# Optimization experiments

Hardware: AMD Instinct MI355X
Metric: run time of the kernel (lower is better)

Reference implementation:

```python
import jax, jax.numpy as jnp
import numpy as np

N = 50000          # num nodes
E = 1_000_000      # num edges
H = 64             # hidden_dim
IMG, TWT, NUMP, CAT = 512, 768, 16, 8
NCLS, NET = 2, 3   # num_classes, num_edge_types


def setup_inputs() -> dict:
    key = jax.random.key(0)
    ks = jax.random.split(key, 40)
    f32 = jnp.float32
    w = lambda k, s: (jax.random.normal(k, s, f32) * 0.02)
    inp = {
        # forward args
        "image": jax.random.normal(ks[0], (N, IMG), f32),
        "tweets": jax.random.normal(ks[1], (N, TWT), f32),
        "num_prop": jax.random.normal(ks[2], (N, NUMP), f32),
        "category": jax.random.normal(ks[3], (N, CAT), f32),
        "edge_index": jax.random.randint(ks[4], (2, E), 0, N, jnp.int32),
        "edge_type": jax.random.randint(ks[5], (E,), 0, NET, jnp.int32),
        # explicit randomness (replaces randn_like / Bernoulli.sample)
        "eps": jax.random.normal(ks[6], (E, H), f32),
        "u": jax.random.uniform(ks[7], (E,), f32),
        # parameters (stored [in, out]; y = x @ W + b)
        "Wi": w(ks[8], (IMG, H)), "bi": jnp.zeros((H,), f32),
        "Wt": w(ks[9], (TWT, H)), "bt": jnp.zeros((H,), f32),
        "Wn": w(ks[10], (NUMP, H)), "bn": jnp.zeros((H,), f32),
        "Wc": w(ks[11], (CAT, H)), "bc": jnp.zeros((H,), f32),
        "Wf": w(ks[12], (4 * H, H)), "bf": jnp.zeros((H,), f32),
        "Eet": w(ks[13], (NET, 2 * H)),              # edge_type_embed
        "Wmu": w(ks[14], (2 * H, H)), "bmu": jnp.zeros((H,), f32),
        "Wlv": w(ks[15], (2 * H, H)), "blv": jnp.zeros((H,), f32),
        "Wm1": w(ks[16], (2 * H, 64)), "bm1": jnp.zeros((64,), f32),
        "Wm2": w(ks[17], (64, 1)), "bm2": jnp.zeros((1,), f32),
        "Wcls": w(ks[18], (H, NCLS)), "bcls": jnp.zeros((NCLS,), f32),
    }
    return inp


def reference(image, tweets, num_prop, category, edge_index, edge_type, eps, u,
              Wi, bi, Wt, bt, Wn, bn, Wc, bc, Wf, bf, Eet,
              Wmu, bmu, Wlv, blv, Wm1, bm1, Wm2, bm2, Wcls, bcls):
    relu = jax.nn.relu
    # encode_user
    img_f = relu(image @ Wi + bi)
    twt_f = relu(tweets @ Wt + bt)
    num_f = relu(num_prop @ Wn + bn)
    cat_f = relu(category @ Wc + bc)
    node_features = relu(jnp.concatenate([img_f, twt_f, num_f, cat_f], -1) @ Wf + bf)  # [N, H]

    src, dst = edge_index[0], edge_index[1]
    u_i, u_j = node_features[src], node_features[dst]          # [E, H] each
    edge_emb = relu(jnp.concatenate([u_i, u_j], -1) + Eet[edge_type])  # [E, 2H]

    # parameterized_gaussian (z unused downstream, kept for fidelity)
    mu = edge_emb @ Wmu + bmu
    log_var = edge_emb @ Wlv + blv
    z = mu + eps * jnp.exp(0.5 * log_var)

    # edge confidence + Bernoulli sample via inverse-CDF with provided uniforms
    logits_e = (relu(edge_emb @ Wm1 + bm1) @ Wm2 + bm2)[:, 0]  # [E]
    p_ij = jax.nn.sigmoid(logits_e)
    s = (u < p_ij).astype(node_features.dtype)                 # trusted-edge indicator, [E]

    # segment-mean of dst features over trusted edges, grouped by src
    sums = jax.ops.segment_sum(u_j * s[:, None], src, num_segments=N)  # [N, H]
    cnt = jax.ops.segment_sum(s, src, num_segments=N)                  # [N]
    agg = jnp.where(cnt[:, None] > 0, sums / jnp.maximum(cnt, 1.0)[:, None], node_features)

    return agg @ Wcls + bcls  # [N, num_classes]
```

## Files before the change

### kernel.cpp

```cpp
#include <hip/hip_runtime.h>
#include <cstdint>

typedef short short8 __attribute__((ext_vector_type(8)));
typedef float f32x4  __attribute__((ext_vector_type(4)));

__device__ __forceinline__ void split2(float x, short& h, short& l) {
  unsigned u  = __float_as_uint(x);
  unsigned rh = u + 0x7FFFu + ((u >> 16) & 1u);
  h = (short)(rh >> 16);
  float hf = __uint_as_float((rh >> 16) << 16);
  float lf = x - hf;
  unsigned ul = __float_as_uint(lf);
  unsigned rl = ul + 0x7FFFu + ((ul >> 16) & 1u);
  l = (short)(rl >> 16);
}

__global__ __launch_bounds__(256) void init_head(int* __restrict__ head, int N)
{
  const int i = blockIdx.x * 256 + threadIdx.x;
  if (i < N) head[i] = -1;
}

__global__ __launch_bounds__(256) void prep_w(
    const float* __restrict__ Wi, const float* __restrict__ Wt,
    const float* __restrict__ Wn, const float* __restrict__ Wc,
    const float* __restrict__ Wf, short* __restrict__ hi, short* __restrict__ lo)
{
  int idx = blockIdx.x * 256 + threadIdx.x;
  if (idx >= 1600 * 64) return;
  int kp = idx >> 6, col = idx & 63;
  const float* W; int K, kloc, base;
  if (kp < 512)       { W = Wi; K = 512; kloc = kp;        base = 0;    }
  else if (kp < 1280) { W = Wt; K = 768; kloc = kp - 512;  base = 512;  }
  else if (kp < 1312) { W = Wn; K = 16;  kloc = kp - 1280; base = 1280; }
  else if (kp < 1344) { W = Wc; K = 8;   kloc = kp - 1312; base = 1312; }
  else                { W = Wf; K = 256; kloc = kp - 1344; base = 1344; }
  float x = (kloc < K) ? W[(size_t)kloc * 64 + col] : 0.f;
  short h, l; split2(x, h, l);
  int s = kloc >> 5;
  int addr = ((s * 4 + (col >> 4)) * 64 + ((col & 15) | (((kloc >> 3) & 3) << 4))) * 8 + (kloc & 7);
  size_t o = (size_t)base * 64 + addr;
  hi[o] = h; lo[o] = l;
}

__global__ __launch_bounds__(256) void gemm_mfma_relu(
    const float* __restrict__ A, int lda, int K, int ksteps,
    const short* __restrict__ Whi, const short* __restrict__ Wlo,
    const float* __restrict__ bias, float* __restrict__ C, int ldc, int M)
{
  __shared__ short Ahi[2][2048];
  __shared__ short Alo[2][2048];
  const int tid = threadIdx.x;
  const int m0  = blockIdx.x * 64;
  const int w   = tid >> 6, l = tid & 63;

  f32x4 acc[4];
#pragma unroll
  for (int n = 0; n < 4; n++) acc[n] = (f32x4){0.f, 0.f, 0.f, 0.f};

  const int srow = tid >> 3;
  const int k0   = (tid & 7) * 4;
  const int i0   = k0 & 7;
  const int kg   = k0 >> 3;

  auto stage = [&](int s, int buf) {
#pragma unroll
    for (int r2 = 0; r2 < 2; r2++) {
      const int row  = srow + r2 * 32;
      const int grow = m0 + row;
      const int k    = s * 32 + k0;
      float4 a = make_float4(0.f, 0.f, 0.f, 0.f);
      if (grow < M && k < K)
        a = *reinterpret_cast<const float4*>(A + (size_t)grow * lda + k);
      unsigned hp0, hp1, lp0, lp1;
      asm("v_cvt_pk_bf16_f32 %0, %1, %2" : "=v"(hp0) : "v"(a.x), "v"(a.y));
      asm("v_cvt_pk_bf16_f32 %0, %1, %2" : "=v"(hp1) : "v"(a.z), "v"(a.w));
      float h0 = __uint_as_float(hp0 << 16);
      float h1 = __uint_as_float(hp0 & 0xFFFF0000u);
      float h2 = __uint_as_float(hp1 << 16);
      float h3 = __uint_as_float(hp1 & 0xFFFF0000u);
      float l0 = a.x - h0, l1 = a.y - h1, l2 = a.z - h2, l3 = a.w - h3;
      asm("v_cvt_pk_bf16_f32 %0, %1, %2" : "=v"(lp0) : "v"(l0), "v"(l1));
      asm("v_cvt_pk_bf16_f32 %0, %1, %2" : "=v"(lp1) : "v"(l2), "v"(l3));
      const int addr = (row >> 4) * 512 + (((row & 15) | (kg << 4)) * 8 + i0);
      *reinterpret_cast<uint2*>(&Ahi[buf][addr]) = make_uint2(hp0, hp1);
      *reinterpret_cast<uint2*>(&Alo[buf][addr]) = make_uint2(lp0, lp1);
    }
  };

  stage(0, 0);
  for (int s = 0; s < ksteps; s++) {
    __syncthreads();
    if (s + 1 < ksteps) stage(s + 1, (s + 1) & 1);
    const int buf = s & 1;
    short8 ahi = *reinterpret_cast<const short8*>(&Ahi[buf][w * 512 + l * 8]);
    short8 alo = *reinterpret_cast<const short8*>(&Alo[buf][w * 512 + l * 8]);
#pragma unroll
    for (int n = 0; n < 4; n++) {
      short8 whi = *reinterpret_cast<const short8*>(&Whi[((size_t)(s * 4 + n)) * 512 + l * 8]);
      short8 wlo = *reinterpret_cast<const short8*>(&Wlo[((size_t)(s * 4 + n)) * 512 + l * 8]);
      acc[n] = __builtin_amdgcn_mfma_f32_16x16x32_bf16(ahi, whi, acc[n], 0, 0, 0);
      acc[n] = __builtin_amdgcn_mfma_f32_16x16x32_bf16(alo, whi, acc[n], 0, 0, 0);
      acc[n] = __builtin_amdgcn_mfma_f32_16x16x32_bf16(ahi, wlo, acc[n], 0, 0, 0);
    }
  }

  const int rb  = m0 + w * 16 + (l >> 4) * 4;
  const int c15 = l & 15;
#pragma unroll
  for (int n = 0; n < 4; n++) {
    const int c = n * 16 + c15;
    const float bb = bias[c];
#pragma unroll
    for (int j = 0; j < 4; j++) {
      const int r = rb + j;
      if (r < M) C[(size_t)r * ldc + c] = fmaxf(acc[n][j] + bb, 0.f);
    }
  }
}

__global__ __launch_bounds__(256) void build_table(
    const float* __restrict__ nf, const float* __restrict__ Eet, int eoff,
    const float* __restrict__ Wm1half, const float* __restrict__ bias,
    float* __restrict__ Tab, int N3)
{
  __shared__ float Es[64][68];
  __shared__ float Ws[64][68];
  const int tid = threadIdx.x;
  const int m0  = blockIdx.x * 64;
  const int ty  = tid >> 4, tx = tid & 15;

  {
    const int r = tid >> 2;
    const int rg = m0 + r;
    const int n = rg / 3;
    const int t = rg - n * 3;
#pragma unroll
    for (int j = 0; j < 4; j++) {
      const int k0 = (tid & 3) * 4 + j * 16;
      float4 v = make_float4(0.f, 0.f, 0.f, 0.f);
      if (rg < N3) {
        float4 x = *reinterpret_cast<const float4*>(nf + (size_t)n * 64 + k0);
        float4 e = *reinterpret_cast<const float4*>(Eet + (size_t)t * 128 + eoff + k0);
        v.x = fmaxf(x.x + e.x, 0.f); v.y = fmaxf(x.y + e.y, 0.f);
        v.z = fmaxf(x.z + e.z, 0.f); v.w = fmaxf(x.w + e.w, 0.f);
      }
      Es[k0 + 0][r] = v.x; Es[k0 + 1][r] = v.y;
      Es[k0 + 2][r] = v.z; Es[k0 + 3][r] = v.w;
    }
  }
  {
    const int kr = tid >> 4, c0 = (tid & 15) * 4;
#pragma unroll
    for (int j = 0; j < 4; j++) {
      const int k = kr + j * 16;
      *reinterpret_cast<float4*>(&Ws[k][c0]) =
          *reinterpret_cast<const float4*>(Wm1half + (size_t)k * 64 + c0);
    }
  }
  __syncthreads();

  float acc[4][4];
#pragma unroll
  for (int i = 0; i < 4; i++)
#pragma unroll
    for (int j = 0; j < 4; j++) acc[i][j] = 0.f;

#pragma unroll 16
  for (int kk = 0; kk < 64; kk++) {
    float4 a = *reinterpret_cast<const float4*>(&Es[kk][ty * 4]);
    float4 w = *reinterpret_cast<const float4*>(&Ws[kk][tx * 4]);
    float av[4] = {a.x, a.y, a.z, a.w};
    float wv[4] = {w.x, w.y, w.z, w.w};
#pragma unroll
    for (int i = 0; i < 4; i++)
#pragma unroll
      for (int j = 0; j < 4; j++)
        acc[i][j] = fmaf(av[i], wv[j], acc[i][j]);
  }

  float4 bv = make_float4(0.f, 0.f, 0.f, 0.f);
  if (bias) bv = *reinterpret_cast<const float4*>(bias + tx * 4);
#pragma unroll
  for (int i = 0; i < 4; i++) {
    const int row = m0 + ty * 4 + i;
    if (row < N3) {
      float4 o = make_float4(acc[i][0] + bv.x, acc[i][1] + bv.y,
                             acc[i][2] + bv.z, acc[i][3] + bv.w);
      *reinterpret_cast<float4*>(Tab + (size_t)row * 64 + tx * 4) = o;
    }
  }
}

__global__ __launch_bounds__(256) void edge_kernel(
    const int* __restrict__ ei, const int* __restrict__ et,
    const float* __restrict__ u,
    const float* __restrict__ Atab, const float* __restrict__ Btab,
    const float* __restrict__ Wm2, const float* __restrict__ bm2,
    int* __restrict__ head, int* __restrict__ nxt, int E)
{
  const int tid = threadIdx.x;
  const int e   = blockIdx.x * 16 + (tid >> 4);
  const int sub = tid & 15;
  if (e >= E) return;

  const int sn = ei[e];
  const int dn = ei[E + e];
  const int t  = et[e];

  float4 a  = *reinterpret_cast<const float4*>(Atab + ((size_t)sn * 3 + t) * 64 + sub * 4);
  float4 b  = *reinterpret_cast<const float4*>(Btab + ((size_t)dn * 3 + t) * 64 + sub * 4);
  float4 wv = *reinterpret_cast<const float4*>(Wm2 + sub * 4);

  float v = fmaxf(a.x + b.x, 0.f) * wv.x;
  v = fmaf(fmaxf(a.y + b.y, 0.f), wv.y, v);
  v = fmaf(fmaxf(a.z + b.z, 0.f), wv.z, v);
  v = fmaf(fmaxf(a.w + b.w, 0.f), wv.w, v);
  v += __shfl_xor(v, 1);
  v += __shfl_xor(v, 2);
  v += __shfl_xor(v, 4);
  v += __shfl_xor(v, 8);

  if (sub == 0) {
    const float p = 1.f / (1.f + expf(-(v + bm2[0])));
    if (u[e] < p) {
      nxt[e] = atomicExch(&head[sn], e);
    }
  }
}

__global__ __launch_bounds__(256) void node_kernel(
    const int* __restrict__ head, const int* __restrict__ nxt,
    const int* __restrict__ ei,
    const float* __restrict__ nf,
    const float* __restrict__ Wcls, const float* __restrict__ bcls,
    float* __restrict__ out, int N, int E)
{
  const int n    = (int)((blockIdx.x * (unsigned)blockDim.x + threadIdx.x) >> 6);
  const int lane = threadIdx.x & 63;
  if (n >= N) return;

  float acc = 0.f;
  int   c   = 0;
  int   e   = head[n];
  while (e >= 0) {
    const int dn = ei[E + e];
    acc += nf[(size_t)dn * 64 + lane];
    c++;
    e = nxt[e];
  }

  const float agg = (c > 0) ? acc / (float)c : nf[(size_t)n * 64 + lane];
  float r0 = agg * Wcls[lane * 2 + 0];
  float r1 = agg * Wcls[lane * 2 + 1];
#pragma unroll
  for (int off = 32; off; off >>= 1) {
    r0 += __shfl_xor(r0, off, 64);
    r1 += __shfl_xor(r1, off, 64);
  }
  if (lane == 0) {
    out[(size_t)n * 2 + 0] = r0 + bcls[0];
    out[(size_t)n * 2 + 1] = r1 + bcls[1];
  }
}

extern "C" void kernel_launch(void* const* d_in, const int* in_sizes, int n_in,
                              void* d_out, int out_size, void* d_ws, size_t ws_size,
                              hipStream_t stream)
{
  const float* image    = (const float*)d_in[0];
  const float* tweets   = (const float*)d_in[1];
  const float* num_prop = (const float*)d_in[2];
  const float* category = (const float*)d_in[3];
  const int*   ei       = (const int*)  d_in[4];
  const int*   et       = (const int*)  d_in[5];
  const float* u        = (const float*)d_in[7];
  const float* Wi  = (const float*)d_in[8],  *bi  = (const float*)d_in[9];
  const float* Wt  = (const float*)d_in[10], *bt  = (const float*)d_in[11];
  const float* Wn  = (const float*)d_in[12], *bn  = (const float*)d_in[13];
  const float* Wc  = (const float*)d_in[14], *bc  = (const float*)d_in[15];
  const float* Wf  = (const float*)d_in[16], *bf  = (const float*)d_in[17];
  const float* Eet = (const float*)d_in[18];
  const float* Wm1 = (const float*)d_in[23], *bm1 = (const float*)d_in[24];
  const float* Wm2 = (const float*)d_in[25], *bm2 = (const float*)d_in[26];
  const float* Wcls= (const float*)d_in[27], *bcls= (const float*)d_in[28];
  float* out = (float*)d_out;

  const int N = in_sizes[0] / 512;
  const int E = in_sizes[5];

  float* ws = (float*)d_ws;
  size_t off = 0;
  float* concat = ws + off;  off += (size_t)N * 256;
  float* nf     = ws + off;  off += (size_t)N * 64;
  float* Atab   = ws + off;  off += (size_t)N * 3 * 64;
  float* Btab   = ws + off;  off += (size_t)N * 3 * 64;
  int*   head   = (int*)(ws + off);  off += (size_t)N;
  int*   nxt    = (int*)(ws + off);  off += (size_t)E;
  short* Wfhi   = (short*)(ws + off);  off += (1600 * 64) / 2;
  short* Wflo   = (short*)(ws + off);  off += (1600 * 64) / 2;

  init_head<<<(N + 255) / 256, 256, 0, stream>>>(head, N);

  prep_w<<<(1600 * 64 + 255) / 256, 256, 0, stream>>>(Wi, Wt, Wn, Wc, Wf, Wfhi, Wflo);

  const int gN = (N + 63) / 64;
  gemm_mfma_relu<<<gN, 256, 0, stream>>>(image,    512, 512, 16, Wfhi + (size_t)0    * 64, Wflo + (size_t)0    * 64, bi, concat + 0,   256, N);
  gemm_mfma_relu<<<gN, 256, 0, stream>>>(tweets,   768, 768, 24, Wfhi + (size_t)512  * 64, Wflo + (size_t)512  * 64, bt, concat + 64,  256, N);
  gemm_mfma_relu<<<gN, 256, 0, stream>>>(num_prop, 16,  16,  1,  Wfhi + (size_t)1280 * 64, Wflo + (size_t)1280 * 64, bn, concat + 128, 256, N);
  gemm_mfma_relu<<<gN, 256, 0, stream>>>(category, 8,   8,   1,  Wfhi + (size_t)1312 * 64, Wflo + (size_t)1312 * 64, bc, concat + 192, 256, N);
  gemm_mfma_relu<<<gN, 256, 0, stream>>>(concat,   256, 256, 8,  Wfhi + (size_t)1344 * 64, Wflo + (size_t)1344 * 64, bf, nf,           64,  N);

  const int N3 = N * 3;
  const int gT = (N3 + 63) / 64;
  build_table<<<gT, 256, 0, stream>>>(nf, Eet, 0,  Wm1,           bm1,     Atab, N3);
  build_table<<<gT, 256, 0, stream>>>(nf, Eet, 64, Wm1 + 64 * 64, nullptr, Btab, N3);

  edge_kernel<<<(E + 15) / 16, 256, 0, stream>>>(ei, et, u, Atab, Btab,
                                                 Wm2, bm2, head, nxt, E);

  node_kernel<<<(N + 3) / 4, 256, 0, stream>>>(head, nxt, ei, nf, Wcls, bcls,
                                               out, N, E);
}
```

Measured before the change: 391.6 us.

## Fuse encoder GEMMs into one kernel and move edge tables to split-bf16 MFMA

The four input-projection GEMMs and the fusion GEMM are merged into one encoder kernel. Each segment's ReLU output is kept in shared memory and immediately multiplied into the fusion accumulator, so the N×256 concat buffer is never written to or read back from global memory. The two FP32 build_table launches become one MFMA kernel using split-bf16 weights prepared by prep_w. The node aggregation also switches to double accumulation for accuracy, which costs FP64 adds in the gather loop.

```diff
diff --git a/kernel.cpp b/kernel.cpp
--- a/kernel.cpp
+++ b/kernel.cpp
@@ -15,6 +15,21 @@
   l = (short)(rl >> 16);
 }
 
+__device__ __forceinline__ void split4(float4 a, uint2& hp, uint2& lp) {
+  unsigned hp0, hp1, lp0, lp1;
+  asm("v_cvt_pk_bf16_f32 %0, %1, %2" : "=v"(hp0) : "v"(a.x), "v"(a.y));
+  asm("v_cvt_pk_bf16_f32 %0, %1, %2" : "=v"(hp1) : "v"(a.z), "v"(a.w));
+  float h0 = __uint_as_float(hp0 << 16);
+  float h1 = __uint_as_float(hp0 & 0xFFFF0000u);
+  float h2 = __uint_as_float(hp1 << 16);
+  float h3 = __uint_as_float(hp1 & 0xFFFF0000u);
+  float l0 = a.x - h0, l1 = a.y - h1, l2 = a.z - h2, l3 = a.w - h3;
+  asm("v_cvt_pk_bf16_f32 %0, %1, %2" : "=v"(lp0) : "v"(l0), "v"(l1));
+  asm("v_cvt_pk_bf16_f32 %0, %1, %2" : "=v"(lp1) : "v"(l2), "v"(l3));
+  hp = make_uint2(hp0, hp1);
+  lp = make_uint2(lp0, lp1);
+}
+
 __global__ __launch_bounds__(256) void init_head(int* __restrict__ head, int N)
 {
   const int i = blockIdx.x * 256 + threadIdx.x;
@@ -24,17 +39,20 @@
 __global__ __launch_bounds__(256) void prep_w(
     const float* __restrict__ Wi, const float* __restrict__ Wt,
     const float* __restrict__ Wn, const float* __restrict__ Wc,
-    const float* __restrict__ Wf, short* __restrict__ hi, short* __restrict__ lo)
+    const float* __restrict__ Wf, const float* __restrict__ Wm1,
+    short* __restrict__ hi, short* __restrict__ lo)
 {
   int idx = blockIdx.x * 256 + threadIdx.x;
-  if (idx >= 1600 * 64) return;
+  if (idx >= 1728 * 64) return;
   int kp = idx >> 6, col = idx & 63;
   const float* W; int K, kloc, base;
-  if (kp < 512)       { W = Wi; K = 512; kloc = kp;        base = 0;    }
-  else if (kp < 1280) { W = Wt; K = 768; kloc = kp - 512;  base = 512;  }
-  else if (kp < 1312) { W = Wn; K = 16;  kloc = kp - 1280; base = 1280; }
-  else if (kp < 1344) { W = Wc; K = 8;   kloc = kp - 1312; base = 1312; }
-  else                { W = Wf; K = 256; kloc = kp - 1344; base = 1344; }
+  if (kp < 512)       { W = Wi;            K = 512; kloc = kp;        base = 0;    }
+  else if (kp < 1280) { W = Wt;            K = 768; kloc = kp - 512;  base = 512;  }
+  else if (kp < 1312) { W = Wn;            K = 16;  kloc = kp - 1280; base = 1280; }
+  else if (kp < 1344) { W = Wc;            K = 8;   kloc = kp - 1312; base = 1312; }
+  else if (kp < 1600) { W = Wf;            K = 256; kloc = kp - 1344; base = 1344; }
+  else if (kp < 1664) { W = Wm1;           K = 64;  kloc = kp - 1600; base = 1600; }
+  else                { W = Wm1 + 64 * 64; K = 64;  kloc = kp - 1664; base = 1664; }
   float x = (kloc < K) ? W[(size_t)kloc * 64 + col] : 0.f;
   short h, l; split2(x, h, l);
   int s = kloc >> 5;
@@ -43,62 +61,193 @@
   hi[o] = h; lo[o] = l;
 }
 
-__global__ __launch_bounds__(256) void gemm_mfma_relu(
-    const float* __restrict__ A, int lda, int K, int ksteps,
+__global__ __launch_bounds__(256) void encoder(
+    const float* __restrict__ image, const float* __restrict__ tweets,
+    const float* __restrict__ nump, const float* __restrict__ catg,
     const short* __restrict__ Whi, const short* __restrict__ Wlo,
-    const float* __restrict__ bias, float* __restrict__ C, int ldc, int M)
+    const float* __restrict__ bi, const float* __restrict__ bt,
+    const float* __restrict__ bn, const float* __restrict__ bc,
+    const float* __restrict__ bf, float* __restrict__ nf, int M)
 {
   __shared__ short Ahi[2][2048];
   __shared__ short Alo[2][2048];
-  const int tid = threadIdx.x;
-  const int m0  = blockIdx.x * 64;
-  const int w   = tid >> 6, l = tid & 63;
-
-  f32x4 acc[4];
-#pragma unroll
-  for (int n = 0; n < 4; n++) acc[n] = (f32x4){0.f, 0.f, 0.f, 0.f};
-
+  __shared__ float htile[64 * 68];
+  const int tid  = threadIdx.x;
+  const int m0   = blockIdx.x * 64;
+  const int w    = tid >> 6, l = tid & 63;
   const int srow = tid >> 3;
   const int k0   = (tid & 7) * 4;
   const int i0   = k0 & 7;
   const int kg   = k0 >> 3;
 
-  auto stage = [&](int s, int buf) {
+  f32x4 acc2[4];
+#pragma unroll
+  for (int n = 0; n < 4; n++) acc2[n] = (f32x4){0.f, 0.f, 0.f, 0.f};
+
+  auto stage = [&](const float* A, int lda, int K, int s, int buf) {
 #pragma unroll
     for (int r2 = 0; r2 < 2; r2++) {
       const int row  = srow + r2 * 32;
       const int grow = m0 + row;
       const int k    = s * 32 + k0;
       float4 a = make_float4(0.f, 0.f, 0.f, 0.f);
-      if (grow < M && k < K)
-        a = *reinterpret_cast<const float4*>(A + (size_t)grow * lda + k);
-      unsigned hp0, hp1, lp0, lp1;
-      asm("v_cvt_pk_bf16_f32 %0, %1, %2" : "=v"(hp0) : "v"(a.x), "v"(a.y));
-      asm("v_cvt_pk_bf16_f32 %0, %1, %2" : "=v"(hp1) : "v"(a.z), "v"(a.w));
-      float h0 = __uint_as_float(hp0 << 16);
-      float h1 = __uint_as_float(hp0 & 0xFFFF0000u);
-      float h2 = __uint_as_float(hp1 << 16);
-      float h3 = __uint_as_float(hp1 & 0xFFFF0000u);
-      float l0 = a.x - h0, l1 = a.y - h1, l2 = a.z - h2, l3 = a.w - h3;
-      asm("v_cvt_pk_bf16_f32 %0, %1, %2" : "=v"(lp0) : "v"(l0), "v"(l1));
-      asm("v_cvt_pk_bf16_f32 %0, %1, %2" : "=v"(lp1) : "v"(l2), "v"(l3));
+      if (grow < M && k < K) {
+        if (k + 3 < K) {
+          a = *reinterpret_cast<const float4*>(A + (size_t)grow * lda + k);
+        } else {
+          a.x = A[(size_t)grow * lda + k];
+        }
+      }
+      uint2 hp, lp; split4(a, hp, lp);
       const int addr = (row >> 4) * 512 + (((row & 15) | (kg << 4)) * 8 + i0);
-      *reinterpret_cast<uint2*>(&Ahi[buf][addr]) = make_uint2(hp0, hp1);
-      *reinterpret_cast<uint2*>(&Alo[buf][addr]) = make_uint2(lp0, lp1);
+      *reinterpret_cast<uint2*>(&Ahi[buf][addr]) = hp;
+      *reinterpret_cast<uint2*>(&Alo[buf][addr]) = lp;
     }
   };
 
-  stage(0, 0);
-  for (int s = 0; s < ksteps; s++) {
+  auto do_segment = [&](const float* A, int lda, int K, int ksteps,
+                        int wstep0, const float* bias, int seg) {
+    f32x4 acc[4];
+#pragma unroll
+    for (int n = 0; n < 4; n++) acc[n] = (f32x4){0.f, 0.f, 0.f, 0.f};
+
+    stage(A, lda, K, 0, 0);
+    for (int s = 0; s < ksteps; s++) {
+      __syncthreads();
+      if (s + 1 < ksteps) stage(A, lda, K, s + 1, (s + 1) & 1);
+      const int buf = s & 1;
+      short8 ahi = *reinterpret_cast<const short8*>(&Ahi[buf][w * 512 + l * 8]);
+      short8 alo = *reinterpret_cast<const short8*>(&Alo[buf][w * 512 + l * 8]);
+#pragma unroll
+      for (int n = 0; n < 4; n++) {
+        short8 whi = *reinterpret_cast<const short8*>(&Whi[((size_t)(wstep0 + s) * 4 + n) * 512 + l * 8]);
+        short8 wlo = *reinterpret_cast<const short8*>(&Wlo[((size_t)(wstep0 + s) * 4 + n) * 512 + l * 8]);
+        acc[n] = __builtin_amdgcn_mfma_f32_16x16x32_bf16(ahi, whi, acc[n], 0, 0, 0);
+        acc[n] = __builtin_amdgcn_mfma_f32_16x16x32_bf16(alo, whi, acc[n], 0, 0, 0);
+        acc[n] = __builtin_amdgcn_mfma_f32_16x16x32_bf16(ahi, wlo, acc[n], 0, 0, 0);
+      }
+    }
     __syncthreads();
-    if (s + 1 < ksteps) stage(s + 1, (s + 1) & 1);
-    const int buf = s & 1;
-    short8 ahi = *reinterpret_cast<const short8*>(&Ahi[buf][w * 512 + l * 8]);
-    short8 alo = *reinterpret_cast<const short8*>(&Alo[buf][w * 512 + l * 8]);
+
 #pragma unroll
     for (int n = 0; n < 4; n++) {
-      short8 whi = *reinterpret_cast<const short8*>(&Whi[((size_t)(s * 4 + n)) * 512 + l * 8]);
-      short8 wlo = *reinterpret_cast<const short8*>(&Wlo[((size_t)(s * 4 + n)) * 512 + l * 8]);
+      const int c  = n * 16 + (l & 15);
+      const float bb = bias[c];
+#pragma unroll
+      for (int j = 0; j < 4; j++) {
+        const int row = w * 16 + (l >> 4) * 4 + j;
+        htile[row * 68 + c] = fmaxf(acc[n][j] + bb, 0.f);
+      }
+    }
+    __syncthreads();
+
+#pragma unroll
+    for (int ks2 = 0; ks2 < 2; ks2++) {
+#pragma unroll
+      for (int r2 = 0; r2 < 2; r2++) {
+        const int row = srow + r2 * 32;
+        float4 a = *reinterpret_cast<const float4*>(&htile[row * 68 + ks2 * 32 + k0]);
+        uint2 hp, lp; split4(a, hp, lp);
+        const int addr = (row >> 4) * 512 + (((row & 15) | (kg << 4)) * 8 + i0);
+        *reinterpret_cast<uint2*>(&Ahi[ks2][addr]) = hp;
+        *reinterpret_cast<uint2*>(&Alo[ks2][addr]) = lp;
+      }
+    }
+    __syncthreads();
+
+#pragma unroll
+    for (int ks2 = 0; ks2 < 2; ks2++) {
+      short8 ahi = *reinterpret_cast<const short8*>(&Ahi[ks2][w * 512 + l * 8]);
+      short8 alo = *reinterpret_cast<const short8*>(&Alo[ks2][w * 512 + l * 8]);
+      const int st = 42 + seg * 2 + ks2;
+#pragma unroll
+      for (int n = 0; n < 4; n++) {
+        short8 whi = *reinterpret_cast<const short8*>(&Whi[((size_t)st * 4 + n) * 512 + l * 8]);
+        short8 wlo = *reinterpret_cast<const short8*>(&Wlo[((size_t)st * 4 + n) * 512 + l * 8]);
+        acc2[n] = __builtin_amdgcn_mfma_f32_16x16x32_bf16(ahi, whi, acc2[n], 0, 0, 0);
+        acc2[n] = __builtin_amdgcn_mfma_f32_16x16x32_bf16(alo, whi, acc2[n], 0, 0, 0);
+        acc2[n] = __builtin_amdgcn_mfma_f32_16x16x32_bf16(ahi, wlo, acc2[n], 0, 0, 0);
+      }
+    }
+    __syncthreads();
+  };
+
+  do_segment(image,  512, 512, 16, 0,  bi, 0);
+  do_segment(tweets, 768, 768, 24, 16, bt, 1);
+  do_segment(nump,   16,  16,  1,  40, bn, 2);
+  do_segment(catg,   8,   8,   1,  41, bc, 3);
+
+  const int rb  = m0 + w * 16 + (l >> 4) * 4;
+  const int c15 = l & 15;
+#pragma unroll
+  for (int n = 0; n < 4; n++) {
+    const int c = n * 16 + c15;
+    const float bb = bf[c];
+#pragma unroll
+    for (int j = 0; j < 4; j++) {
+      const int r = rb + j;
+      if (r < M) nf[(size_t)r * 64 + c] = fmaxf(acc2[n][j] + bb, 0.f);
+    }
+  }
+}
+
+__global__ __launch_bounds__(256) void table_kernel(
+    const float* __restrict__ nf, const float* __restrict__ Eet,
+    const short* __restrict__ Whi, const short* __restrict__ Wlo,
+    const float* __restrict__ bm1,
+    float* __restrict__ Atab, float* __restrict__ Btab, int N3, int gT)
+{
+  const bool isB    = (int)blockIdx.x >= gT;
+  const int  m0     = (isB ? (int)blockIdx.x - gT : (int)blockIdx.x) * 64;
+  const int  eoff   = isB ? 64 : 0;
+  const int  wstep0 = isB ? 52 : 50;
+  float*     Tab    = isB ? Btab : Atab;
+
+  __shared__ short Ahi[2][2048];
+  __shared__ short Alo[2][2048];
+  const int tid  = threadIdx.x;
+  const int w    = tid >> 6, l = tid & 63;
+  const int srow = tid >> 3;
+  const int k0   = (tid & 7) * 4;
+  const int i0   = k0 & 7;
+  const int kg   = k0 >> 3;
+
+#pragma unroll
+  for (int ks2 = 0; ks2 < 2; ks2++) {
+#pragma unroll
+    for (int r2 = 0; r2 < 2; r2++) {
+      const int row = srow + r2 * 32;
+      const int rg  = m0 + row;
+      float4 v = make_float4(0.f, 0.f, 0.f, 0.f);
+      if (rg < N3) {
+        const int n = rg / 3;
+        const int t = rg - n * 3;
+        const int k = ks2 * 32 + k0;
+        float4 x = *reinterpret_cast<const float4*>(&nf[(size_t)n * 64 + k]);
+        float4 e = *reinterpret_cast<const float4*>(&Eet[(size_t)t * 128 + eoff + k]);
+        v.x = fmaxf(x.x + e.x, 0.f); v.y = fmaxf(x.y + e.y, 0.f);
+        v.z = fmaxf(x.z + e.z, 0.f); v.w = fmaxf(x.w + e.w, 0.f);
+      }
+      uint2 hp, lp; split4(v, hp, lp);
+      const int addr = (row >> 4) * 512 + (((row & 15) | (kg << 4)) * 8 + i0);
+      *reinterpret_cast<uint2*>(&Ahi[ks2][addr]) = hp;
+      *reinterpret_cast<uint2*>(&Alo[ks2][addr]) = lp;
+    }
+  }
+  __syncthreads();
+
+  f32x4 acc[4];
+#pragma unroll
+  for (int n = 0; n < 4; n++) acc[n] = (f32x4){0.f, 0.f, 0.f, 0.f};
+
+#pragma unroll
+  for (int ks2 = 0; ks2 < 2; ks2++) {
+    short8 ahi = *reinterpret_cast<const short8*>(&Ahi[ks2][w * 512 + l * 8]);
+    short8 alo = *reinterpret_cast<const short8*>(&Alo[ks2][w * 512 + l * 8]);
+#pragma unroll
+    for (int n = 0; n < 4; n++) {
+      short8 whi = *reinterpret_cast<const short8*>(&Whi[((size_t)(wstep0 + ks2) * 4 + n) * 512 + l * 8]);
+      short8 wlo = *reinterpret_cast<const short8*>(&Wlo[((size_t)(wstep0 + ks2) * 4 + n) * 512 + l * 8]);
       acc[n] = __builtin_amdgcn_mfma_f32_16x16x32_bf16(ahi, whi, acc[n], 0, 0, 0);
       acc[n] = __builtin_amdgcn_mfma_f32_16x16x32_bf16(alo, whi, acc[n], 0, 0, 0);
       acc[n] = __builtin_amdgcn_mfma_f32_16x16x32_bf16(ahi, wlo, acc[n], 0, 0, 0);
@@ -110,84 +259,11 @@
 #pragma unroll
   for (int n = 0; n < 4; n++) {
     const int c = n * 16 + c15;
-    const float bb = bias[c];
+    const float bb = isB ? 0.f : bm1[c];
 #pragma unroll
     for (int j = 0; j < 4; j++) {
       const int r = rb + j;
-      if (r < M) C[(size_t)r * ldc + c] = fmaxf(acc[n][j] + bb, 0.f);
-    }
-  }
-}
-
-__global__ __launch_bounds__(256) void build_table(
-    const float* __restrict__ nf, const float* __restrict__ Eet, int eoff,
-    const float* __restrict__ Wm1half, const float* __restrict__ bias,
-    float* __restrict__ Tab, int N3)
-{
-  __shared__ float Es[64][68];
-  __shared__ float Ws[64][68];
-  const int tid = threadIdx.x;
-  const int m0  = blockIdx.x * 64;
-  const int ty  = tid >> 4, tx = tid & 15;
-
-  {
-    const int r = tid >> 2;
-    const int rg = m0 + r;
-    const int n = rg / 3;
-    const int t = rg - n * 3;
-#pragma unroll
-    for (int j = 0; j < 4; j++) {
-      const int k0 = (tid & 3) * 4 + j * 16;
-      float4 v = make_float4(0.f, 0.f, 0.f, 0.f);
-      if (rg < N3) {
-        float4 x = *reinterpret_cast<const float4*>(nf + (size_t)n * 64 + k0);
-        float4 e = *reinterpret_cast<const float4*>(Eet + (size_t)t * 128 + eoff + k0);
-        v.x = fmaxf(x.x + e.x, 0.f); v.y = fmaxf(x.y + e.y, 0.f);
-        v.z = fmaxf(x.z + e.z, 0.f); v.w = fmaxf(x.w + e.w, 0.f);
-      }
-      Es[k0 + 0][r] = v.x; Es[k0 + 1][r] = v.y;
-      Es[k0 + 2][r] = v.z; Es[k0 + 3][r] = v.w;
-    }
-  }
-  {
-    const int kr = tid >> 4, c0 = (tid & 15) * 4;
-#pragma unroll
-    for (int j = 0; j < 4; j++) {
-      const int k = kr + j * 16;
-      *reinterpret_cast<float4*>(&Ws[k][c0]) =
-          *reinterpret_cast<const float4*>(Wm1half + (size_t)k * 64 + c0);
-    }
-  }
-  __syncthreads();
-
-  float acc[4][4];
-#pragma unroll
-  for (int i = 0; i < 4; i++)
-#pragma unroll
-    for (int j = 0; j < 4; j++) acc[i][j] = 0.f;
-
-#pragma unroll 16
-  for (int kk = 0; kk < 64; kk++) {
-    float4 a = *reinterpret_cast<const float4*>(&Es[kk][ty * 4]);
-    float4 w = *reinterpret_cast<const float4*>(&Ws[kk][tx * 4]);
-    float av[4] = {a.x, a.y, a.z, a.w};
-    float wv[4] = {w.x, w.y, w.z, w.w};
-#pragma unroll
-    for (int i = 0; i < 4; i++)
-#pragma unroll
-      for (int j = 0; j < 4; j++)
-        acc[i][j] = fmaf(av[i], wv[j], acc[i][j]);
-  }
-
-  float4 bv = make_float4(0.f, 0.f, 0.f, 0.f);
-  if (bias) bv = *reinterpret_cast<const float4*>(bias + tx * 4);
-#pragma unroll
-  for (int i = 0; i < 4; i++) {
-    const int row = m0 + ty * 4 + i;
-    if (row < N3) {
-      float4 o = make_float4(acc[i][0] + bv.x, acc[i][1] + bv.y,
-                             acc[i][2] + bv.z, acc[i][3] + bv.w);
-      *reinterpret_cast<float4*>(Tab + (size_t)row * 64 + tx * 4) = o;
+      if (r < N3) Tab[(size_t)r * 64 + c] = acc[n][j] + bb;
     }
   }
 }
@@ -240,17 +316,17 @@
   const int lane = threadIdx.x & 63;
   if (n >= N) return;
 
-  float acc = 0.f;
-  int   c   = 0;
-  int   e   = head[n];
+  double acc = 0.0;
+  int    c   = 0;
+  int    e   = head[n];
   while (e >= 0) {
     const int dn = ei[E + e];
-    acc += nf[(size_t)dn * 64 + lane];
+    acc += (double)nf[(size_t)dn * 64 + lane];
     c++;
     e = nxt[e];
   }
 
-  const float agg = (c > 0) ? acc / (float)c : nf[(size_t)n * 64 + lane];
+  const float agg = (c > 0) ? (float)(acc / (double)c) : nf[(size_t)n * 64 + lane];
   float r0 = agg * Wcls[lane * 2 + 0];
   float r1 = agg * Wcls[lane * 2 + 1];
 #pragma unroll
@@ -291,30 +367,27 @@
 
   float* ws = (float*)d_ws;
   size_t off = 0;
-  float* concat = ws + off;  off += (size_t)N * 256;
   float* nf     = ws + off;  off += (size_t)N * 64;
   float* Atab   = ws + off;  off += (size_t)N * 3 * 64;
   float* Btab   = ws + off;  off += (size_t)N * 3 * 64;
   int*   head   = (int*)(ws + off);  off += (size_t)N;
   int*   nxt    = (int*)(ws + off);  off += (size_t)E;
-  short* Wfhi   = (short*)(ws + off);  off += (1600 * 64) / 2;
-  short* Wflo   = (short*)(ws + off);  off += (1600 * 64) / 2;
+  short* Wfhi   = (short*)(ws + off);  off += (1728 * 64) / 2;
+  short* Wflo   = (short*)(ws + off);  off += (1728 * 64) / 2;
 
   init_head<<<(N + 255) / 256, 256, 0, stream>>>(head, N);
 
-  prep_w<<<(1600 * 64 + 255) / 256, 256, 0, stream>>>(Wi, Wt, Wn, Wc, Wf, Wfhi, Wflo);
+  prep_w<<<(1728 * 64 + 255) / 256, 256, 0, stream>>>(Wi, Wt, Wn, Wc, Wf, Wm1,
+                                                      Wfhi, Wflo);
 
   const int gN = (N + 63) / 64;
-  gemm_mfma_relu<<<gN, 256, 0, stream>>>(image,    512, 512, 16, Wfhi + (size_t)0    * 64, Wflo + (size_t)0    * 64, bi, concat + 0,   256, N);
-  gemm_mfma_relu<<<gN, 256, 0, stream>>>(tweets,   768, 768, 24, Wfhi + (size_t)512  * 64, Wflo + (size_t)512  * 64, bt, concat + 64,  256, N);
-  gemm_mfma_relu<<<gN, 256, 0, stream>>>(num_prop, 16,  16,  1,  Wfhi + (size_t)1280 * 64, Wflo + (size_t)1280 * 64, bn, concat + 128, 256, N);
-  gemm_mfma_relu<<<gN, 256, 0, stream>>>(category, 8,   8,   1,  Wfhi + (size_t)1312 * 64, Wflo + (size_t)1312 * 64, bc, concat + 192, 256, N);
-  gemm_mfma_relu<<<gN, 256, 0, stream>>>(concat,   256, 256, 8,  Wfhi + (size_t)1344 * 64, Wflo + (size_t)1344 * 64, bf, nf,           64,  N);
+  encoder<<<gN, 256, 0, stream>>>(image, tweets, num_prop, category,
+                                  Wfhi, Wflo, bi, bt, bn, bc, bf, nf, N);
 
   const int N3 = N * 3;
   const int gT = (N3 + 63) / 64;
-  build_table<<<gT, 256, 0, stream>>>(nf, Eet, 0,  Wm1,           bm1,     Atab, N3);
-  build_table<<<gT, 256, 0, stream>>>(nf, Eet, 64, Wm1 + 64 * 64, nullptr, Btab, N3);
+  table_kernel<<<2 * gT, 256, 0, stream>>>(nf, Eet, Wfhi, Wflo, bm1,
+                                           Atab, Btab, N3, gT);
 
   edge_kernel<<<(E + 15) / 16, 256, 0, stream>>>(ei, et, u, Atab, Btab,
                                                  Wm2, bm2, head, nxt, E);
```

Result: faster. 328.8 us (-16.0%).
